# Optimization experiments

Measured on AMD Instinct MI355X. Metric: run time of the kernel, lower is better.

## Reference

```python
import jax, jax.numpy as jnp
import numpy as np

B, N, K = 2, 8192, 16
D1, D2, OUT = 128, 256, 128


def setup_inputs() -> dict:
    key = jax.random.key(0)
    ks = jax.random.split(key, 6)
    return {
        "xyz1": jax.random.normal(ks[0], (B, N, 3), dtype=jnp.float32),
        "xyz2": jax.random.normal(ks[1], (B, N, 3), dtype=jnp.float32),
        "points1": jax.random.normal(ks[2], (B, N, D1), dtype=jnp.float32),
        "points2": jax.random.normal(ks[3], (B, N, D2), dtype=jnp.float32),
        # Conv1d(k=1) == pointwise linear: weight [OUT, D1+D2], bias [OUT]
        "W": jax.random.normal(ks[4], (OUT, D1 + D2), dtype=jnp.float32) / np.sqrt(D1 + D2).astype(np.float32),
        "b": jax.random.normal(ks[5], (OUT,), dtype=jnp.float32) * 0.01,
        "nsample": K,
    }


def reference(xyz1, xyz2, points1, points2, W, b, nsample):
    Bb, Nn, _ = xyz1.shape
    # squared pairwise distances, queries=xyz2, keys=xyz1 -> [B, N, N]
    d2 = (jnp.sum(xyz2 * xyz2, -1)[:, :, None]
          + jnp.sum(xyz1 * xyz1, -1)[:, None, :]
          - 2.0 * jnp.einsum('bsc,bnc->bsn', xyz2, xyz1))
    neg_vals, idx = jax.lax.top_k(-d2, nsample)          # K nearest
    dists = -neg_vals                                     # [B, N, K] sq dists
    recip = 1.0 / (dists + 1e-8)
    weight = recip / jnp.sum(recip, axis=2, keepdims=True)  # inverse-dist weights
    # gather neighbor features from points2: [B, N, K, D2]
    g = jnp.take_along_axis(points2, idx.reshape(Bb, Nn * nsample)[:, :, None], axis=1)
    g = g.reshape(Bb, Nn, nsample, -1)
    interp = jnp.sum(g * weight[..., None], axis=2)       # [B, N, D2]
    cat = jnp.concatenate([points1, interp], axis=-1)     # [B, N, D1+D2]
    # Conv1d(kernel=1) over channel dim
    return jnp.einsum('bnc,oc->bno', cat, W) + b
```

## Files before the change

### kernel.cpp

```cpp
#include <hip/hip_runtime.h>
#include <stdint.h>

#define BQ   2
#define NQ   8192
#define D1Q  128
#define D2Q  256
#define OUTQ 128
#define CATQ 384
#define KQ   16

__device__ __forceinline__ ushort f2bf(float f) {
    uint32_t u = __float_as_uint(f);
    return (ushort)((u + 0x7FFFu + ((u >> 16) & 1u)) >> 16);
}
__device__ __forceinline__ float bf2f(ushort h) {
    return __uint_as_float((uint32_t)h << 16);
}

typedef __attribute__((ext_vector_type(8))) short short8v;
typedef __attribute__((ext_vector_type(4))) float f32x4v;

__global__ void prep_kernel(const float* __restrict__ W,
                            ushort* __restrict__ Wfh, ushort* __restrict__ Wfl,
                            const float* __restrict__ xyz1,
                            float4* __restrict__ xyz1n) {
    int flat = blockIdx.x * 256 + threadIdx.x;
    if (flat < CATQ * OUTQ) {
        int r    = flat & 7;
        int lane = (flat >> 3) & 63;
        int ctk  = flat >> 9;
        int ct   = ctk & 7;
        int kt   = ctk >> 3;
        int o = ct * 16 + (lane & 15);
        int k = kt * 32 + (lane >> 4) * 8 + r;
        float v  = W[o * CATQ + k];
        ushort h = f2bf(v);
        Wfh[flat] = h;
        Wfl[flat] = f2bf(v - bf2f(h));
    }
    if (flat < BQ * NQ) {
        float x = xyz1[flat * 3 + 0];
        float y = xyz1[flat * 3 + 1];
        float z = xyz1[flat * 3 + 2];
        float n;
        {
            #pragma clang fp contract(off)
            float px = x * x, py = y * y, pz = z * z;
            n = (px + py) + pz;
        }
        xyz1n[flat] = make_float4(x, y, z, n);
    }
}

__device__ __forceinline__ void fma4(float4& acc, float a, const float4& w) {
    acc.x = fmaf(a, w.x, acc.x);
    acc.y = fmaf(a, w.y, acc.y);
    acc.z = fmaf(a, w.z, acc.z);
    acc.w = fmaf(a, w.w, acc.w);
}

__device__ __forceinline__ float npy_d2(float4 pt, float qx, float qy, float qz,
                                        float s2) {
    #pragma clang fp contract(off)
    float d0  = pt.x * qx;
    float dot = fmaf(pt.y, qy, d0);
    dot       = fmaf(pt.z, qz, dot);
    float tt  = s2 + pt.w;
    return tt - 2.0f * dot;
}

__device__ __forceinline__ float red_r(float4 pt, float qx, float qy, float qz) {
    float dot = fmaf(pt.z, qz, fmaf(pt.y, qy, pt.x * qx));
    return fmaf(-2.0f, dot, pt.w);
}
#define RED_MARGIN 1e-3f

__device__ __forceinline__ uint64_t sort64(uint64_t x, int lane) {
    #pragma unroll
    for (int k = 2; k <= 64; k <<= 1) {
        #pragma unroll
        for (int j = k >> 1; j > 0; j >>= 1) {
            uint64_t p = __shfl_xor((unsigned long long)x, j, 64);
            bool keep_min = (((lane & j) == 0) == ((lane & k) == 0));
            bool pless    = p < x;
            x = (pless == keep_min) ? p : x;
        }
    }
    return x;
}

__global__ __launch_bounds__(256, 5) void fused_kernel(
        const float4* __restrict__ xyz1n, const float* __restrict__ xyz2,
        const float* __restrict__ points1, const float* __restrict__ points2,
        const ushort* __restrict__ Wfh, const ushort* __restrict__ Wfl,
        const float* __restrict__ bias, float* __restrict__ out) {
    __shared__ __align__(16) char smem[32768];
    float4*   xyzt4 = (float4*)smem;
    uint64_t* wball = (uint64_t*)(smem + 16384);
    ushort*   cat_h = (ushort*)smem;
    ushort*   cat_l = (ushort*)(smem + 12544);

    const int tid   = threadIdx.x;
    const int lane  = tid & 63;
    const int w     = tid >> 6;
    const int qbase = blockIdx.x * 16 + w * 4;
    const int b     = (blockIdx.x * 16) >> 13;

    float qx[4], qy[4], qz[4], s2[4];
    #pragma unroll
    for (int j = 0; j < 4; ++j) {
        const float* qp = xyz2 + (size_t)(qbase + j) * 3;
        qx[j] = qp[0]; qy[j] = qp[1]; qz[j] = qp[2];
        {
            #pragma clang fp contract(off)
            float px = qx[j] * qx[j], py = qy[j] * qy[j], pz = qz[j] * qz[j];
            s2[j] = (px + py) + pz;
        }
    }

    const float4* xb = xyz1n + (size_t)b * NQ;

    float mn[4];
    #pragma unroll
    for (int j = 0; j < 4; ++j) mn[j] = __uint_as_float(0x7F800000u);

    for (int tile = 0; tile < 4; ++tile) {
        __syncthreads();
        {
            const float4* s4 = xb + tile * 1024;
            #pragma unroll
            for (int v = tid; v < 1024; v += 256) xyzt4[v] = s4[v];
        }
        __syncthreads();
        #pragma unroll 4
        for (int s = 0; s < 16; ++s) {
            float4 pt = xyzt4[s * 64 + lane];
            #pragma unroll
            for (int j = 0; j < 4; ++j)
                mn[j] = fminf(mn[j], red_r(pt, qx[j], qy[j], qz[j]));
        }
    }

    float that[4];
    #pragma unroll
    for (int j = 0; j < 4; ++j) {
        float x = mn[j];
        #pragma unroll
        for (int k = 2; k <= 64; k <<= 1) {
            #pragma unroll
            for (int jj = k >> 1; jj > 0; jj >>= 1) {
                float px = __shfl_xor(x, jj, 64);
                bool keep_min = (((lane & jj) == 0) == ((lane & k) == 0));
                float mnv = fminf(x, px), mxv = fmaxf(x, px);
                x = keep_min ? mnv : mxv;
            }
        }
        that[j] = s2[j] + __shfl(x, 15, 64) + RED_MARGIN;
    }

    uint32_t cnt[4] = {0u, 0u, 0u, 0u};
    for (int tt = 0; tt < 8; ++tt) {
        const int tile = (3 + tt) & 7;
        if (tt > 0) {
            __syncthreads();
            const float4* s4 = xb + tile * 1024;
            #pragma unroll
            for (int v = tid; v < 1024; v += 256) xyzt4[v] = s4[v];
            __syncthreads();
        }
        const uint32_t base = (uint32_t)tile * 1024u;
        #pragma unroll 4
        for (int s = 0; s < 16; ++s) {
            float4 pt = xyzt4[s * 64 + lane];
            const uint32_t pidx = base + (uint32_t)(s * 64 + lane);
            #pragma unroll
            for (int j = 0; j < 4; ++j) {
                float d2 = npy_d2(pt, qx[j], qy[j], qz[j], s2[j]);
                bool  v  = (d2 <= that[j]);
                uint64_t mask = __ballot((int)v);
                if (mask != 0ull) {
                    if (v) {
                        uint32_t below = __builtin_amdgcn_mbcnt_hi(
                            (uint32_t)(mask >> 32),
                            __builtin_amdgcn_mbcnt_lo((uint32_t)mask, 0u));
                        uint32_t pos    = cnt[j] + below;
                        uint32_t bits   = __float_as_uint(d2);
                        uint32_t mapped = bits ^ (0x80000000u |
                                          (uint32_t)((int32_t)bits >> 31));
                        if (pos < 128u)
                            wball[(w * 4 + j) * 128 + pos] =
                                ((uint64_t)mapped << 32) | (uint64_t)pidx;
                    }
                    cnt[j] += (uint32_t)__popcll(mask);
                }
            }
        }
    }

    int   myidxA[4];
    float mywgtA[4];
    #pragma unroll
    for (int j = 0; j < 4; ++j) {
        const uint64_t* wb = wball + (size_t)(w * 4 + j) * 128;
        const uint32_t c = cnt[j];
        uint64_t mykey;
        if (c <= 64u) {
            uint64_t k0 = (lane < (int)c) ? wb[lane] : ~0ull;
            mykey = sort64(k0, lane);
        } else {
            uint32_t cc = c > 128u ? 128u : c;
            uint64_t k0 = wb[lane];
            uint64_t k1 = (lane + 64 < (int)cc) ? wb[lane + 64] : ~0ull;
            k0 = sort64(k0, lane);
            k1 = sort64(k1, lane);
            uint64_t t1 = __shfl((unsigned long long)k1, lane & 15, 64);
            uint64_t km = (lane < 16) ? k0 : ((lane < 32) ? t1 : ~0ull);
            mykey = sort64(km, lane);
        }
        uint32_t mhi   = (uint32_t)(mykey >> 32);
        uint32_t rbits = (mhi & 0x80000000u) ? (mhi ^ 0x80000000u) : ~mhi;
        float    d2w   = __uint_as_float(rbits);
        myidxA[j] = (int)(uint32_t)(mykey & 0xFFFFFFFFull);
        float recip = (lane < KQ) ? (1.0f / (d2w + 1e-8f)) : 0.0f;
        float tot = recip;
        #pragma unroll
        for (int sh = 1; sh < 16; sh <<= 1) tot += __shfl_xor(tot, sh, 64);
        mywgtA[j] = recip / tot;
    }

    __syncthreads();

    const float* p2b = points2 + (size_t)b * NQ * D2Q;
    #pragma unroll
    for (int j = 0; j < 4; ++j) {
        const int qi = w * 4 + j;
        if (lane < 32) {
            float4 p = ((const float4*)(points1 + (size_t)(qbase + j) * D1Q))[lane];
            ushort4 hv, lv;
            hv.x = f2bf(p.x); lv.x = f2bf(p.x - bf2f(hv.x));
            hv.y = f2bf(p.y); lv.y = f2bf(p.y - bf2f(hv.y));
            hv.z = f2bf(p.z); lv.z = f2bf(p.z - bf2f(hv.z));
            hv.w = f2bf(p.w); lv.w = f2bf(p.w - bf2f(hv.w));
            *(ushort4*)&cat_h[qi * 392 + lane * 4] = hv;
            *(ushort4*)&cat_l[qi * 392 + lane * 4] = lv;
        }
        float4 acc = make_float4(0.f, 0.f, 0.f, 0.f);
        #pragma unroll
        for (int k = 0; k < KQ; ++k) {
            int   kk = __builtin_amdgcn_readlane(myidxA[j], k);
            float wk = __uint_as_float((uint32_t)__builtin_amdgcn_readlane(
                           (int)__float_as_uint(mywgtA[j]), k));
            float4 row = ((const float4*)(p2b + (size_t)kk * D2Q))[lane];
            acc.x = fmaf(wk, row.x, acc.x);
            acc.y = fmaf(wk, row.y, acc.y);
            acc.z = fmaf(wk, row.z, acc.z);
            acc.w = fmaf(wk, row.w, acc.w);
        }
        {
            ushort4 hv, lv;
            hv.x = f2bf(acc.x); lv.x = f2bf(acc.x - bf2f(hv.x));
            hv.y = f2bf(acc.y); lv.y = f2bf(acc.y - bf2f(hv.y));
            hv.z = f2bf(acc.z); lv.z = f2bf(acc.z - bf2f(hv.z));
            hv.w = f2bf(acc.w); lv.w = f2bf(acc.w - bf2f(hv.w));
            *(ushort4*)&cat_h[qi * 392 + D1Q + lane * 4] = hv;
            *(ushort4*)&cat_l[qi * 392 + D1Q + lane * 4] = lv;
        }
    }
    __syncthreads();

    {
        const int arow = lane & 15;
        const int koff = (lane >> 4) * 8;
        const int ct0  = w * 2;
        f32x4v acc0 = {0.f, 0.f, 0.f, 0.f};
        f32x4v acc1 = {0.f, 0.f, 0.f, 0.f};
        #pragma unroll 4
        for (int kt = 0; kt < 12; ++kt) {
            short8v ah = *(const short8v*)&cat_h[arow * 392 + kt * 32 + koff];
            short8v al = *(const short8v*)&cat_l[arow * 392 + kt * 32 + koff];
            const ushort* bhp = Wfh + ((size_t)(kt * 8 + ct0) * 64 + lane) * 8;
            const ushort* blp = Wfl + ((size_t)(kt * 8 + ct0) * 64 + lane) * 8;
            short8v bh0 = *(const short8v*)bhp;
            short8v bl0 = *(const short8v*)blp;
            short8v bh1 = *(const short8v*)(bhp + 512);
            short8v bl1 = *(const short8v*)(blp + 512);
            acc0 = __builtin_amdgcn_mfma_f32_16x16x32_bf16(ah, bh0, acc0, 0, 0, 0);
            acc0 = __builtin_amdgcn_mfma_f32_16x16x32_bf16(al, bh0, acc0, 0, 0, 0);
            acc0 = __builtin_amdgcn_mfma_f32_16x16x32_bf16(ah, bl0, acc0, 0, 0, 0);
            acc1 = __builtin_amdgcn_mfma_f32_16x16x32_bf16(ah, bh1, acc1, 0, 0, 0);
            acc1 = __builtin_amdgcn_mfma_f32_16x16x32_bf16(al, bh1, acc1, 0, 0, 0);
            acc1 = __builtin_amdgcn_mfma_f32_16x16x32_bf16(ah, bl1, acc1, 0, 0, 0);
        }
        const int col0 = ct0 * 16 + (lane & 15);
        const int row0 = blockIdx.x * 16 + (lane >> 4) * 4;
        const float bv0 = bias[col0];
        const float bv1 = bias[col0 + 16];
        #pragma unroll
        for (int r = 0; r < 4; ++r) {
            out[(size_t)(row0 + r) * OUTQ + col0]      = acc0[r] + bv0;
            out[(size_t)(row0 + r) * OUTQ + col0 + 16] = acc1[r] + bv1;
        }
    }
}

extern "C" void kernel_launch(void* const* d_in, const int* in_sizes, int n_in,
                              void* d_out, int out_size, void* d_ws, size_t ws_size,
                              hipStream_t stream) {
    const float* xyz1    = (const float*)d_in[0];
    const float* xyz2    = (const float*)d_in[1];
    const float* points1 = (const float*)d_in[2];
    const float* points2 = (const float*)d_in[3];
    const float* W       = (const float*)d_in[4];
    const float* bias    = (const float*)d_in[5];

    ushort* Wfh   = (ushort*)d_ws;
    ushort* Wfl   = (ushort*)((char*)d_ws + 98304);
    float4* xyz1n = (float4*)((char*)d_ws + 196608);

    prep_kernel<<<192, 256, 0, stream>>>(W, Wfh, Wfl, xyz1, xyz1n);
    fused_kernel<<<(BQ * NQ) / 16, 256, 0, stream>>>(
        xyz1n, xyz2, points1, points2, Wfh, Wfl, bias, (float*)d_out);
}
```

Before: 162.9 us.

## Morton-sort points and cull distance groups by bounding box for KNN

Adds preprocessing kernels that bin xyz1 and xyz2 into a 16^3 Morton grid, build a histogram and prefix sum, scatter both point sets into spatially sorted order, and compute a bounding box for every 64-point group. The fused kernel now takes its top-16 threshold from a local 2048-point window rather than all 8192 points. It then scans only the point groups whose box lower bound falls within the threshold, and writes outputs back through the original query indices. This removes most of the brute-force N×N distance work, at the cost of five extra small launches, atomics, indirect gathers and lower occupancy.

```diff
diff --git a/kernel.cpp b/kernel.cpp
--- a/kernel.cpp
+++ b/kernel.cpp
@@ -9,6 +9,20 @@
 #define CATQ 384
 #define KQ   16
 
+#define NBIN 4096
+#define RED_MARGIN 1e-3f
+#define LB_MARGIN  1e-2f
+
+#define WS_WFH   0
+#define WS_WFL   98304
+#define WS_HIST  196608
+#define WS_SPXYZ 262144
+#define WS_QSXYZ 524288
+#define WS_SPIDX 786432
+#define WS_QSIDX 819200
+#define WS_GBLO  851968
+#define WS_GBHI  856064
+
 __device__ __forceinline__ ushort f2bf(float f) {
     uint32_t u = __float_as_uint(f);
     return (ushort)((u + 0x7FFFu + ((u >> 16) & 1u)) >> 16);
@@ -20,10 +34,21 @@
 typedef __attribute__((ext_vector_type(8))) short short8v;
 typedef __attribute__((ext_vector_type(4))) float f32x4v;
 
-__global__ void prep_kernel(const float* __restrict__ W,
-                            ushort* __restrict__ Wfh, ushort* __restrict__ Wfl,
-                            const float* __restrict__ xyz1,
-                            float4* __restrict__ xyz1n) {
+__device__ __forceinline__ int mort_bin(float x, float y, float z) {
+    int bx = (int)((x + 5.0f) * 1.6f); bx = bx < 0 ? 0 : (bx > 15 ? 15 : bx);
+    int by = (int)((y + 5.0f) * 1.6f); by = by < 0 ? 0 : (by > 15 ? 15 : by);
+    int bz = (int)((z + 5.0f) * 1.6f); bz = bz < 0 ? 0 : (bz > 15 ? 15 : bz);
+    int k = 0;
+    #pragma unroll
+    for (int t = 0; t < 4; ++t)
+        k |= (((bx >> t) & 1) << (3 * t)) | (((by >> t) & 1) << (3 * t + 1)) |
+             (((bz >> t) & 1) << (3 * t + 2));
+    return k;
+}
+
+__global__ void prep_w_kernel(const float* __restrict__ W,
+                              ushort* __restrict__ Wfh, ushort* __restrict__ Wfl,
+                              uint32_t* __restrict__ hist) {
     int flat = blockIdx.x * 256 + threadIdx.x;
     if (flat < CATQ * OUTQ) {
         int r    = flat & 7;
@@ -38,25 +63,108 @@
         Wfh[flat] = h;
         Wfl[flat] = f2bf(v - bf2f(h));
     }
-    if (flat < BQ * NQ) {
-        float x = xyz1[flat * 3 + 0];
-        float y = xyz1[flat * 3 + 1];
-        float z = xyz1[flat * 3 + 2];
+    if (flat < 4 * NBIN) hist[flat] = 0u;
+}
+
+__global__ void hist_kernel(const float* __restrict__ xyz1,
+                            const float* __restrict__ xyz2,
+                            uint32_t* __restrict__ hist) {
+    int i = blockIdx.x * 256 + threadIdx.x;
+    if (i < BQ * NQ) {
+        int batch = i >> 13;
+        const float* p = xyz1 + (size_t)i * 3;
+        int bin = mort_bin(p[0], p[1], p[2]);
+        atomicAdd(&hist[batch * NBIN + bin], 1u);
+    } else {
+        int j = i - BQ * NQ;
+        int batch = j >> 13;
+        const float* p = xyz2 + (size_t)j * 3;
+        int bin = mort_bin(p[0], p[1], p[2]);
+        atomicAdd(&hist[(2 + batch) * NBIN + bin], 1u);
+    }
+}
+
+__global__ void prefix_kernel(uint32_t* __restrict__ hist) {
+    __shared__ uint32_t sc[1024];
+    uint32_t* h = hist + (size_t)blockIdx.x * NBIN;
+    int t = threadIdx.x;
+    uint32_t v0 = h[4 * t], v1 = h[4 * t + 1], v2 = h[4 * t + 2], v3 = h[4 * t + 3];
+    uint32_t s = v0 + v1 + v2 + v3;
+    sc[t] = s;
+    __syncthreads();
+    for (int d = 1; d < 1024; d <<= 1) {
+        uint32_t x = (t >= d) ? sc[t - d] : 0u;
+        __syncthreads();
+        sc[t] += x;
+        __syncthreads();
+    }
+    uint32_t excl = sc[t] - s;
+    h[4 * t]     = excl;
+    h[4 * t + 1] = excl + v0;
+    h[4 * t + 2] = excl + v0 + v1;
+    h[4 * t + 3] = excl + v0 + v1 + v2;
+}
+
+__global__ void scatter_kernel(const float* __restrict__ xyz1,
+                               const float* __restrict__ xyz2,
+                               uint32_t* __restrict__ hist,
+                               float4* __restrict__ sp_xyzn,
+                               float4* __restrict__ qs_xyzw,
+                               ushort* __restrict__ sp_idx,
+                               ushort* __restrict__ qs_idx) {
+    int i = blockIdx.x * 256 + threadIdx.x;
+    if (i < BQ * NQ) {
+        int batch = i >> 13;
+        const float* p = xyz1 + (size_t)i * 3;
+        float x = p[0], y = p[1], z = p[2];
+        int bin = mort_bin(x, y, z);
+        uint32_t pos = atomicAdd(&hist[batch * NBIN + bin], 1u);
         float n;
         {
             #pragma clang fp contract(off)
             float px = x * x, py = y * y, pz = z * z;
             n = (px + py) + pz;
         }
-        xyz1n[flat] = make_float4(x, y, z, n);
-    }
-}
-
-__device__ __forceinline__ void fma4(float4& acc, float a, const float4& w) {
-    acc.x = fmaf(a, w.x, acc.x);
-    acc.y = fmaf(a, w.y, acc.y);
-    acc.z = fmaf(a, w.z, acc.z);
-    acc.w = fmaf(a, w.w, acc.w);
+        sp_xyzn[batch * NQ + pos] = make_float4(x, y, z, n);
+        sp_idx[batch * NQ + pos]  = (ushort)(i & (NQ - 1));
+    } else {
+        int j = i - BQ * NQ;
+        int batch = j >> 13;
+        const float* p = xyz2 + (size_t)j * 3;
+        float x = p[0], y = p[1], z = p[2];
+        int bin = mort_bin(x, y, z);
+        uint32_t pos = atomicAdd(&hist[(2 + batch) * NBIN + bin], 1u);
+        float s2;
+        {
+            #pragma clang fp contract(off)
+            float px = x * x, py = y * y, pz = z * z;
+            s2 = (px + py) + pz;
+        }
+        qs_xyzw[batch * NQ + pos] = make_float4(x, y, z, s2);
+        qs_idx[batch * NQ + pos]  = (ushort)(j & (NQ - 1));
+    }
+}
+
+__global__ void gbox_kernel(const float4* __restrict__ sp_xyzn,
+                            float4* __restrict__ gblo, float4* __restrict__ gbhi) {
+    int g = blockIdx.x;
+    int lane = threadIdx.x;
+    float4 pt = sp_xyzn[(size_t)g * 64 + lane];
+    float lx = pt.x, ly = pt.y, lz = pt.z;
+    float hx = pt.x, hy = pt.y, hz = pt.z;
+    #pragma unroll
+    for (int d = 1; d < 64; d <<= 1) {
+        lx = fminf(lx, __shfl_xor(lx, d, 64));
+        ly = fminf(ly, __shfl_xor(ly, d, 64));
+        lz = fminf(lz, __shfl_xor(lz, d, 64));
+        hx = fmaxf(hx, __shfl_xor(hx, d, 64));
+        hy = fmaxf(hy, __shfl_xor(hy, d, 64));
+        hz = fmaxf(hz, __shfl_xor(hz, d, 64));
+    }
+    if (lane == 0) {
+        gblo[g] = make_float4(lx, ly, lz, 0.f);
+        gbhi[g] = make_float4(hx, hy, hz, 0.f);
+    }
 }
 
 __device__ __forceinline__ float npy_d2(float4 pt, float qx, float qy, float qz,
@@ -73,7 +181,6 @@
     float dot = fmaf(pt.z, qz, fmaf(pt.y, qy, pt.x * qx));
     return fmaf(-2.0f, dot, pt.w);
 }
-#define RED_MARGIN 1e-3f
 
 __device__ __forceinline__ uint64_t sort64(uint64_t x, int lane) {
     #pragma unroll
@@ -89,45 +196,75 @@
     return x;
 }
 
-__global__ __launch_bounds__(256, 5) void fused_kernel(
-        const float4* __restrict__ xyz1n, const float* __restrict__ xyz2,
+__global__ __launch_bounds__(256, 4) void fused_kernel(
+        const float4* __restrict__ sp_xyzn, const ushort* __restrict__ sp_idx,
+        const float4* __restrict__ qs_xyzw, const ushort* __restrict__ qs_idx,
         const float* __restrict__ points1, const float* __restrict__ points2,
         const ushort* __restrict__ Wfh, const ushort* __restrict__ Wfl,
-        const float* __restrict__ bias, float* __restrict__ out) {
-    __shared__ __align__(16) char smem[32768];
+        const float* __restrict__ bias,
+        const float4* __restrict__ gblo, const float4* __restrict__ gbhi,
+        float* __restrict__ out) {
+    __shared__ __align__(16) char smem[33792];
     float4*   xyzt4 = (float4*)smem;
     uint64_t* wball = (uint64_t*)(smem + 16384);
+    ushort*   pidm  = (ushort*)(smem + 32768);
+    ushort*   slist = (ushort*)(smem + 33280);
+    ushort*   qsl   = (ushort*)(smem + 33536);
+    uint32_t* scntp = (uint32_t*)(smem + 33568);
+    float4*   qbl   = (float4*)(smem + 33584);
+    float4*   qbh   = (float4*)(smem + 33648);
+    float*    thmaxA= (float*)(smem + 33712);
     ushort*   cat_h = (ushort*)smem;
     ushort*   cat_l = (ushort*)(smem + 12544);
 
     const int tid   = threadIdx.x;
     const int lane  = tid & 63;
     const int w     = tid >> 6;
-    const int qbase = blockIdx.x * 16 + w * 4;
-    const int b     = (blockIdx.x * 16) >> 13;
+    const int blk   = blockIdx.x;
+    const int b     = blk >> 9;
+    const int qslot = (blk & 511) * 16;
+
+    if (tid == 0) *scntp = 0u;
+    if (tid < 16) qsl[tid] = qs_idx[b * NQ + qslot + tid];
 
     float qx[4], qy[4], qz[4], s2[4];
+    int   oqi[4];
     #pragma unroll
     for (int j = 0; j < 4; ++j) {
-        const float* qp = xyz2 + (size_t)(qbase + j) * 3;
-        qx[j] = qp[0]; qy[j] = qp[1]; qz[j] = qp[2];
-        {
-            #pragma clang fp contract(off)
-            float px = qx[j] * qx[j], py = qy[j] * qy[j], pz = qz[j] * qz[j];
-            s2[j] = (px + py) + pz;
-        }
-    }
-
-    const float4* xb = xyz1n + (size_t)b * NQ;
+        float4 q = qs_xyzw[(size_t)b * NQ + qslot + w * 4 + j];
+        qx[j] = q.x; qy[j] = q.y; qz[j] = q.z; s2[j] = q.w;
+        oqi[j] = (int)qs_idx[b * NQ + qslot + w * 4 + j];
+    }
+    {
+        float blx = qx[0], bly = qy[0], blz = qz[0];
+        float bhx = qx[0], bhy = qy[0], bhz = qz[0];
+        #pragma unroll
+        for (int j = 1; j < 4; ++j) {
+            blx = fminf(blx, qx[j]); bly = fminf(bly, qy[j]); blz = fminf(blz, qz[j]);
+            bhx = fmaxf(bhx, qx[j]); bhy = fmaxf(bhy, qy[j]); bhz = fmaxf(bhz, qz[j]);
+        }
+        if (lane == 0) {
+            qbl[w] = make_float4(blx, bly, blz, 0.f);
+            qbh[w] = make_float4(bhx, bhy, bhz, 0.f);
+        }
+    }
+
+    const float4* spb = sp_xyzn + (size_t)b * NQ;
+    const ushort* spi = sp_idx  + (size_t)b * NQ;
+
+    int wstart = qslot + 8 - 1024;
+    if (wstart < 0) wstart = 0;
+    if (wstart > NQ - 2048) wstart = NQ - 2048;
+    wstart &= ~63;
 
     float mn[4];
     #pragma unroll
     for (int j = 0; j < 4; ++j) mn[j] = __uint_as_float(0x7F800000u);
 
-    for (int tile = 0; tile < 4; ++tile) {
+    for (int tile = 0; tile < 2; ++tile) {
         __syncthreads();
         {
-            const float4* s4 = xb + tile * 1024;
+            const float4* s4 = spb + wstart + tile * 1024;
             #pragma unroll
             for (int v = tid; v < 1024; v += 256) xyzt4[v] = s4[v];
         }
@@ -157,22 +294,52 @@
         }
         that[j] = s2[j] + __shfl(x, 15, 64) + RED_MARGIN;
     }
+    {
+        float tm = fmaxf(fmaxf(that[0], that[1]), fmaxf(that[2], that[3]));
+        if (lane == 0) thmaxA[w] = tm;
+    }
+    __syncthreads();
+
+    if (tid < 128) {
+        float4 gl = gblo[b * 128 + tid];
+        float4 gh = gbhi[b * 128 + tid];
+        float qlx = fminf(fminf(qbl[0].x, qbl[1].x), fminf(qbl[2].x, qbl[3].x));
+        float qly = fminf(fminf(qbl[0].y, qbl[1].y), fminf(qbl[2].y, qbl[3].y));
+        float qlz = fminf(fminf(qbl[0].z, qbl[1].z), fminf(qbl[2].z, qbl[3].z));
+        float qhx = fmaxf(fmaxf(qbh[0].x, qbh[1].x), fmaxf(qbh[2].x, qbh[3].x));
+        float qhy = fmaxf(fmaxf(qbh[0].y, qbh[1].y), fmaxf(qbh[2].y, qbh[3].y));
+        float qhz = fmaxf(fmaxf(qbh[0].z, qbh[1].z), fmaxf(qbh[2].z, qbh[3].z));
+        float tmax = fmaxf(fmaxf(thmaxA[0], thmaxA[1]),
+                           fmaxf(thmaxA[2], thmaxA[3]));
+        float dx = fmaxf(fmaxf(qlx - gh.x, gl.x - qhx), 0.f);
+        float dy = fmaxf(fmaxf(qly - gh.y, gl.y - qhy), 0.f);
+        float dz = fmaxf(fmaxf(qlz - gh.z, gl.z - qhz), 0.f);
+        float lb = dx * dx;
+        lb = fmaf(dy, dy, lb);
+        lb = fmaf(dz, dz, lb);
+        if (lb <= tmax + LB_MARGIN) {
+            uint32_t p = atomicAdd(scntp, 1u);
+            slist[p] = (ushort)tid;
+        }
+    }
+    __syncthreads();
+    const int scnt = (int)*scntp;
 
     uint32_t cnt[4] = {0u, 0u, 0u, 0u};
-    for (int tt = 0; tt < 8; ++tt) {
-        const int tile = (3 + tt) & 7;
-        if (tt > 0) {
-            __syncthreads();
-            const float4* s4 = xb + tile * 1024;
-            #pragma unroll
-            for (int v = tid; v < 1024; v += 256) xyzt4[v] = s4[v];
-            __syncthreads();
-        }
-        const uint32_t base = (uint32_t)tile * 1024u;
-        #pragma unroll 4
-        for (int s = 0; s < 16; ++s) {
-            float4 pt = xyzt4[s * 64 + lane];
-            const uint32_t pidx = base + (uint32_t)(s * 64 + lane);
+    for (int c0 = 0; c0 < scnt; c0 += 4) {
+        __syncthreads();
+        {
+            int which = c0 + (tid >> 6);
+            if (which < scnt) {
+                int off = (int)slist[which] * 64 + (tid & 63);
+                xyzt4[tid] = spb[off];
+                pidm[tid]  = spi[off];
+            }
+        }
+        __syncthreads();
+        const int nch = (scnt - c0) < 4 ? (scnt - c0) : 4;
+        for (int k = 0; k < nch; ++k) {
+            float4 pt = xyzt4[k * 64 + lane];
             #pragma unroll
             for (int j = 0; j < 4; ++j) {
                 float d2 = npy_d2(pt, qx[j], qy[j], qz[j], s2[j]);
@@ -187,9 +354,11 @@
                         uint32_t bits   = __float_as_uint(d2);
                         uint32_t mapped = bits ^ (0x80000000u |
                                           (uint32_t)((int32_t)bits >> 31));
-                        if (pos < 128u)
+                        if (pos < 128u) {
+                            uint32_t pidx = (uint32_t)pidm[k * 64 + lane];
                             wball[(w * 4 + j) * 128 + pos] =
                                 ((uint64_t)mapped << 32) | (uint64_t)pidx;
+                        }
                     }
                     cnt[j] += (uint32_t)__popcll(mask);
                 }
@@ -235,7 +404,8 @@
     for (int j = 0; j < 4; ++j) {
         const int qi = w * 4 + j;
         if (lane < 32) {
-            float4 p = ((const float4*)(points1 + (size_t)(qbase + j) * D1Q))[lane];
+            float4 p = ((const float4*)(points1 +
+                        (size_t)(b * NQ + oqi[j]) * D1Q))[lane];
             ushort4 hv, lv;
             hv.x = f2bf(p.x); lv.x = f2bf(p.x - bf2f(hv.x));
             hv.y = f2bf(p.y); lv.y = f2bf(p.y - bf2f(hv.y));
@@ -291,14 +461,16 @@
             acc1 = __builtin_amdgcn_mfma_f32_16x16x32_bf16(al, bh1, acc1, 0, 0, 0);
             acc1 = __builtin_amdgcn_mfma_f32_16x16x32_bf16(ah, bl1, acc1, 0, 0, 0);
         }
-        const int col0 = ct0 * 16 + (lane & 15);
-        const int row0 = blockIdx.x * 16 + (lane >> 4) * 4;
+        const int col0   = ct0 * 16 + (lane & 15);
+        const int r0slot = (lane >> 4) * 4;
         const float bv0 = bias[col0];
         const float bv1 = bias[col0 + 16];
         #pragma unroll
         for (int r = 0; r < 4; ++r) {
-            out[(size_t)(row0 + r) * OUTQ + col0]      = acc0[r] + bv0;
-            out[(size_t)(row0 + r) * OUTQ + col0 + 16] = acc1[r] + bv1;
+            int oq = (int)qsl[r0slot + r];
+            size_t rowoff = (size_t)(b * NQ + oq) * OUTQ;
+            out[rowoff + col0]      = acc0[r] + bv0;
+            out[rowoff + col0 + 16] = acc1[r] + bv1;
         }
     }
 }
@@ -313,11 +485,24 @@
     const float* W       = (const float*)d_in[4];
     const float* bias    = (const float*)d_in[5];
 
-    ushort* Wfh   = (ushort*)d_ws;
-    ushort* Wfl   = (ushort*)((char*)d_ws + 98304);
-    float4* xyz1n = (float4*)((char*)d_ws + 196608);
-
-    prep_kernel<<<192, 256, 0, stream>>>(W, Wfh, Wfl, xyz1, xyz1n);
+    char* ws = (char*)d_ws;
+    ushort*   Wfh     = (ushort*)(ws + WS_WFH);
+    ushort*   Wfl     = (ushort*)(ws + WS_WFL);
+    uint32_t* hist    = (uint32_t*)(ws + WS_HIST);
+    float4*   sp_xyzn = (float4*)(ws + WS_SPXYZ);
+    float4*   qs_xyzw = (float4*)(ws + WS_QSXYZ);
+    ushort*   sp_idx  = (ushort*)(ws + WS_SPIDX);
+    ushort*   qs_idx  = (ushort*)(ws + WS_QSIDX);
+    float4*   gblo    = (float4*)(ws + WS_GBLO);
+    float4*   gbhi    = (float4*)(ws + WS_GBHI);
+
+    prep_w_kernel<<<192, 256, 0, stream>>>(W, Wfh, Wfl, hist);
+    hist_kernel<<<128, 256, 0, stream>>>(xyz1, xyz2, hist);
+    prefix_kernel<<<4, 1024, 0, stream>>>(hist);
+    scatter_kernel<<<128, 256, 0, stream>>>(xyz1, xyz2, hist,
+                                            sp_xyzn, qs_xyzw, sp_idx, qs_idx);
+    gbox_kernel<<<256, 64, 0, stream>>>(sp_xyzn, gblo, gbhi);
     fused_kernel<<<(BQ * NQ) / 16, 256, 0, stream>>>(
-        xyz1n, xyz2, points1, points2, Wfh, Wfl, bias, (float*)d_out);
-}
+        sp_xyzn, sp_idx, qs_xyzw, qs_idx, points1, points2,
+        Wfh, Wfl, bias, gblo, gbhi, (float*)d_out);
+}
```

After: 164.3 us. About the same (+0.9%).
